# Optimization experiments

Measured on AMD Instinct MI355X. Metric: run time of the kernel, lower is better.

Reference implementation:

```python
import jax, jax.numpy as jnp
import numpy as np

N = 500_000      # number of gaussians
F = 32           # grid feature dim (WavePlaneField.feat_dim)
R = 128          # plane resolution
W = 256          # MLP width
BOUNDS = 1.6     # scene aabb half-extent (args.bounds)


def setup_inputs() -> dict:
    key = jax.random.key(0)
    ks = jax.random.split(key, 16)
    s = lambda d: 1.0 / np.sqrt(d)
    return {
        "rays_pts_emb": jax.random.normal(ks[0], (N, 3), jnp.float32),
        "rotations_emb": jax.random.normal(ks[1], (N, 4), jnp.float32),
        "scale_emb": jax.random.uniform(ks[2], (N, 3), jnp.float32),
        "shs_emb": jax.random.normal(ks[3], (N, 16, 3), jnp.float32),
        "view_dir": jax.random.normal(ks[4], (N, 3), jnp.float32),
        "time_emb": jax.random.uniform(ks[5], (N, 1), jnp.float32),
        "h_emb": jax.random.normal(ks[6], (N, 2), jnp.float32),
        # multiplicative k-planes: init near 1 so products are well-scaled
        "space_planes": 1.0 + 0.1 * jax.random.normal(ks[7], (3, R, R, F), jnp.float32),
        "time_planes": 1.0 + 0.1 * jax.random.normal(ks[8], (3, R, R, F), jnp.float32),
        "w_enc": s(F) * jax.random.normal(ks[9], (F, W), jnp.float32),
        "b_enc": jnp.zeros((W,), jnp.float32),
        "w1": s(W) * jax.random.normal(ks[10], (W, W), jnp.float32),
        "b1": jnp.zeros((W,), jnp.float32),
        "w2": s(W) * jax.random.normal(ks[11], (W, 16 * 3), jnp.float32),
        "b2": jnp.zeros((16 * 3,), jnp.float32),
    }


def _interp2d(plane, u, v):
    """Bilinear sample plane [R,R,F] at normalized coords u,v in [0,1]. -> [N,F]"""
    Rr = plane.shape[0]
    x = jnp.clip(u, 0.0, 1.0) * (Rr - 1)
    y = jnp.clip(v, 0.0, 1.0) * (Rr - 1)
    x0 = jnp.clip(jnp.floor(x), 0, Rr - 2).astype(jnp.int32)
    y0 = jnp.clip(jnp.floor(y), 0, Rr - 2).astype(jnp.int32)
    fx = (x - x0)[:, None]
    fy = (y - y0)[:, None]
    p00 = plane[y0, x0]
    p01 = plane[y0, x0 + 1]
    p10 = plane[y0 + 1, x0]
    p11 = plane[y0 + 1, x0 + 1]
    return (p00 * (1 - fx) + p01 * fx) * (1 - fy) + (p10 * (1 - fx) + p11 * fx) * fy


def _covariance(scale, rotation):
    """3DGS: L = R(q) @ diag(s); cov = L L^T; return 6 unique entries [N,6]."""
    q = rotation / jnp.linalg.norm(rotation, axis=-1, keepdims=True)
    r, x, y, z = q[:, 0], q[:, 1], q[:, 2], q[:, 3]
    Rm = jnp.stack([
        jnp.stack([1 - 2 * (y * y + z * z), 2 * (x * y - r * z), 2 * (x * z + r * y)], -1),
        jnp.stack([2 * (x * y + r * z), 1 - 2 * (x * x + z * z), 2 * (y * z - r * x)], -1),
        jnp.stack([2 * (x * z - r * y), 2 * (y * z + r * x), 1 - 2 * (x * x + y * y)], -1),
    ], axis=1)  # [N,3,3]
    L = Rm * scale[:, None, :]                      # R @ diag(s)
    cov = jnp.einsum('nij,nkj->nik', L, L)          # L @ L^T
    return jnp.stack([cov[:, 0, 0], cov[:, 0, 1], cov[:, 0, 2],
                      cov[:, 1, 1], cov[:, 1, 2], cov[:, 2, 2]], axis=-1)


def reference(rays_pts_emb, rotations_emb, scale_emb, shs_emb, view_dir, time_emb,
              h_emb, space_planes, time_planes, w_enc, b_enc, w1, b1, w2, b2):
    # quaternion -> covariance (passed into grid in original; grid lookup itself
    # only needs positions/time, so symm is computed but unused downstream)
    symm = _covariance(scale_emb, rotations_emb)

    pts = rays_pts_emb[:, :3]
    pn = jnp.clip(pts / BOUNDS, -1.0, 1.0) * 0.5 + 0.5  # aabb-normalize to [0,1]
    xn, yn, zn = pn[:, 0], pn[:, 1], pn[:, 2]
    t = jnp.clip(time_emb[:, 0], 0.0, 1.0)

    space = (_interp2d(space_planes[0], xn, yn)
             * _interp2d(space_planes[1], xn, zn)
             * _interp2d(space_planes[2], yn, zn))          # [N,F]
    spacetime = (_interp2d(time_planes[0], xn, t)
                 * _interp2d(time_planes[1], yn, t)
                 * _interp2d(time_planes[2], zn, t))        # [N,F]

    feat = (space * spacetime) @ w_enc + b_enc              # spacetime_enc (Linear only)
    h = jax.nn.relu(feat) @ w1 + b1                         # shs_deform MLP
    d = jax.nn.relu(h) @ w2 + b2                            # [N,48]
    shs = shs_emb + d.reshape(-1, 16, 3)

    del symm  # original forward discards covariance after grid query
    return (rays_pts_emb, rotations_emb, h_emb[:, 0:1], shs)
```

## Files before the change

### kernel.cpp

```cpp
#include <hip/hip_runtime.h>
#include <hip/hip_fp16.h>

#define NPTS 500000
#define RPLANE 128
#define FDIM 32
#define PLSZ (RPLANE * RPLANE * FDIM)

typedef __bf16 bfx8 __attribute__((ext_vector_type(8)));
typedef float f32x4 __attribute__((ext_vector_type(4)));

__device__ __forceinline__ unsigned short f2bf(float f) {
    unsigned int u = __builtin_bit_cast(unsigned int, f);
    unsigned int r = (u + 0x7FFFu + ((u >> 16) & 1u)) >> 16;
    return (unsigned short)r;
}

__device__ __forceinline__ unsigned pk2(float a, float b) {
    return (unsigned)f2bf(a) | ((unsigned)f2bf(b) << 16);
}

__device__ __forceinline__ __half2 u2h(unsigned u) {
    return __builtin_bit_cast(__half2, u);
}

__device__ __forceinline__ bfx8 asfrag(uint4 v) {
    return __builtin_bit_cast(bfx8, v);
}

__device__ __forceinline__ uint4 convD(unsigned e0, unsigned e1, unsigned o0,
                                       unsigned o1, int a0, int a1, bool sel) {
    uint4 W;
    int x, y;
    x = __builtin_amdgcn_ds_bpermute(a0, (int)e0);
    y = __builtin_amdgcn_ds_bpermute(a0, (int)o0);
    W.x = (unsigned)(sel ? y : x);
    x = __builtin_amdgcn_ds_bpermute(a0, (int)e1);
    y = __builtin_amdgcn_ds_bpermute(a0, (int)o1);
    W.y = (unsigned)(sel ? y : x);
    x = __builtin_amdgcn_ds_bpermute(a1, (int)e0);
    y = __builtin_amdgcn_ds_bpermute(a1, (int)o0);
    W.z = (unsigned)(sel ? y : x);
    x = __builtin_amdgcn_ds_bpermute(a1, (int)e1);
    y = __builtin_amdgcn_ds_bpermute(a1, (int)o1);
    W.w = (unsigned)(sel ? y : x);
    return W;
}

__global__ void prep_all(const float* __restrict__ wenc, const float* __restrict__ w1,
                         const float* __restrict__ w2, const float* __restrict__ spf,
                         const float* __restrict__ tpf,
                         unsigned short* __restrict__ wf, __half* __restrict__ ph) {
    const int WTOT = 86016;
    const int PTOT = 6 * PLSZ;
    const int total = WTOT + PTOT;
    for (int i = blockIdx.x * blockDim.x + threadIdx.x; i < total;
         i += gridDim.x * blockDim.x) {
        if (i < WTOT) {
            const float* W;
            unsigned short* dst;
            int K, Ncols, idx;
            if (i < 8192)       { W = wenc; K = 32;  Ncols = 256; idx = i;         dst = wf; }
            else if (i < 73728) { W = w1;   K = 256; Ncols = 256; idx = i - 8192;  dst = wf + 8192; }
            else                { W = w2;   K = 256; Ncols = 48;  idx = i - 73728; dst = wf + 73728; }
            int j = idx & 7;
            int l = (idx >> 3) & 63;
            int b = idx >> 9;
            int KS = K >> 5;
            int ct = b / KS;
            int ks = b - ct * KS;
            int k = ks * 32 + ((l >> 4) << 3) + j;
            int col = ct * 16 + (l & 15);
            dst[idx] = f2bf(W[(size_t)k * Ncols + col]);
        } else {
            int j = i - WTOT;
            float v = (j < 3 * PLSZ) ? spf[j] : tpf[j - 3 * PLSZ];
            ph[j] = __float2half(v);
        }
    }
}

__global__ void pass_copy(const float* __restrict__ rays, const float* __restrict__ rot,
                          const float* __restrict__ h, float* __restrict__ out) {
    const int total = NPTS * 8;
    for (int i = blockIdx.x * blockDim.x + threadIdx.x; i < total; i += gridDim.x * blockDim.x) {
        float v;
        if (i < NPTS * 3) v = rays[i];
        else if (i < NPTS * 7) v = rot[i - NPTS * 3];
        else v = h[(i - NPTS * 7) * 2];
        out[i] = v;
    }
}

__global__ __launch_bounds__(256, 2) void fused4(
    const float* __restrict__ rays, const float* __restrict__ tme,
    const float* __restrict__ shs, const __half* __restrict__ ph,
    const unsigned short* __restrict__ wf,
    const float* __restrict__ benc, const float* __restrict__ b1v,
    const float* __restrict__ b2v, float* __restrict__ out) {
    const int tid = threadIdx.x;
    const int wid = tid >> 6;
    const int lane = tid & 63;
    const int p0 = blockIdx.x * 128 + wid * 32;
    if (p0 >= NPTS) return;
    const int g = lane >> 4;
    const int c = lane & 15;
    const int f0 = g << 3;
    const int a0 = 4 * (32 * (g & 1) + c);
    const int a1 = a0 + 64;
    const bool sel = (g >> 1) != 0;

    bfx8 act1[2];
#pragma unroll
    for (int pt = 0; pt < 2; ++pt) {
        int p = p0 + pt * 16 + c;
        float px = rays[p * 3 + 0], py = rays[p * 3 + 1], pz = rays[p * 3 + 2];
        const float inv = 0.625f;
        float xn = fminf(fmaxf(px * inv, -1.f), 1.f) * 0.5f + 0.5f;
        float yn = fminf(fmaxf(py * inv, -1.f), 1.f) * 0.5f + 0.5f;
        float zn = fminf(fmaxf(pz * inv, -1.f), 1.f) * 0.5f + 0.5f;
        float tt = fminf(fmaxf(tme[p], 0.f), 1.f);
        float c4[4] = {xn, yn, zn, tt};
        int i0[4];
        float fr[4];
#pragma unroll
        for (int cc = 0; cc < 4; ++cc) {
            float x = c4[cc] * 127.0f;
            float xf = fminf(floorf(x), 126.0f);
            i0[cc] = (int)xf;
            fr[cc] = x - xf;
        }
        const int uc[6] = {0, 0, 1, 0, 1, 2};
        const int vc[6] = {1, 2, 2, 3, 3, 3};
        __half2 g2[4];
#pragma unroll
        for (int pl = 0; pl < 6; ++pl) {
            int x0 = i0[uc[pl]], y0 = i0[vc[pl]];
            float fx = fr[uc[pl]], fy = fr[vc[pl]];
            const __half* base = ph + (size_t)pl * PLSZ + ((y0 * RPLANE + x0) << 5) + f0;
            uint4 q00 = *(const uint4*)base;
            uint4 q01 = *(const uint4*)(base + FDIM);
            uint4 q10 = *(const uint4*)(base + RPLANE * FDIM);
            uint4 q11 = *(const uint4*)(base + RPLANE * FDIM + FDIM);
            __half2 wa = __float2half2_rn((1.f - fx) * (1.f - fy));
            __half2 wb = __float2half2_rn(fx * (1.f - fy));
            __half2 wc = __float2half2_rn((1.f - fx) * fy);
            __half2 wd = __float2half2_rn(fx * fy);
            unsigned qa[4] = {q00.x, q00.y, q00.z, q00.w};
            unsigned qb[4] = {q01.x, q01.y, q01.z, q01.w};
            unsigned qc[4] = {q10.x, q10.y, q10.z, q10.w};
            unsigned qd[4] = {q11.x, q11.y, q11.z, q11.w};
#pragma unroll
            for (int i = 0; i < 4; ++i) {
                __half2 r = __hmul2(u2h(qa[i]), wa);
                r = __hfma2(u2h(qb[i]), wb, r);
                r = __hfma2(u2h(qc[i]), wc, r);
                r = __hfma2(u2h(qd[i]), wd, r);
                g2[i] = (pl == 0) ? r : __hmul2(g2[i], r);
            }
        }
        uint4 av;
        {
            float2 v0 = __half22float2(g2[0]);
            float2 v1 = __half22float2(g2[1]);
            float2 v2 = __half22float2(g2[2]);
            float2 v3 = __half22float2(g2[3]);
            av.x = pk2(v0.x, v0.y);
            av.y = pk2(v1.x, v1.y);
            av.z = pk2(v2.x, v2.y);
            av.w = pk2(v3.x, v3.y);
        }
        act1[pt] = asfrag(av);
    }

    uint4 act2[2][8];
    {
        uint4 wA = *(const uint4*)(wf + 0 * 512 + lane * 8);
        uint4 wB;
        unsigned stE[2][2];
#pragma unroll
        for (int ct = 0; ct < 16; ++ct) {
            uint4 cur = (ct & 1) ? wB : wA;
            if (ct < 15) {
                uint4 nx = *(const uint4*)(wf + (size_t)(ct + 1) * 512 + lane * 8);
                if (ct & 1) wA = nx; else wB = nx;
            }
            float4 b4 = *(const float4*)(benc + 16 * ct + 4 * g);
            float bb[4] = {b4.x, b4.y, b4.z, b4.w};
#pragma unroll
            for (int pt = 0; pt < 2; ++pt) {
                f32x4 z = {0.f, 0.f, 0.f, 0.f};
                f32x4 d = __builtin_amdgcn_mfma_f32_16x16x32_bf16(asfrag(cur), act1[pt], z, 0, 0, 0);
                float v0 = fmaxf(d[0] + bb[0], 0.f);
                float v1 = fmaxf(d[1] + bb[1], 0.f);
                float v2 = fmaxf(d[2] + bb[2], 0.f);
                float v3 = fmaxf(d[3] + bb[3], 0.f);
                unsigned Q0 = pk2(v0, v1), Q1 = pk2(v2, v3);
                if ((ct & 1) == 0) {
                    stE[pt][0] = Q0; stE[pt][1] = Q1;
                } else {
                    act2[pt][ct >> 1] = convD(stE[pt][0], stE[pt][1], Q0, Q1, a0, a1, sel);
                }
            }
        }
    }

    uint4 act3[2][8];
    {
        const unsigned short* w1f = wf + 8192;
        uint4 bufA[8], bufB[8];
#pragma unroll
        for (int ks = 0; ks < 8; ++ks)
            bufA[ks] = *(const uint4*)(w1f + (size_t)ks * 512 + lane * 8);
        unsigned stE[2][2];
#pragma unroll
        for (int ct = 0; ct < 16; ++ct) {
            if (ct < 15) {
#pragma unroll
                for (int ks = 0; ks < 8; ++ks) {
                    uint4 nx = *(const uint4*)(w1f + (size_t)((ct + 1) * 8 + ks) * 512 + lane * 8);
                    if (ct & 1) bufA[ks] = nx; else bufB[ks] = nx;
                }
            }
            float4 b4 = *(const float4*)(b1v + 16 * ct + 4 * g);
            float bb[4] = {b4.x, b4.y, b4.z, b4.w};
#pragma unroll
            for (int pt = 0; pt < 2; ++pt) {
                f32x4 acc = {0.f, 0.f, 0.f, 0.f};
#pragma unroll
                for (int ks = 0; ks < 8; ++ks) {
                    uint4 w = (ct & 1) ? bufB[ks] : bufA[ks];
                    acc = __builtin_amdgcn_mfma_f32_16x16x32_bf16(asfrag(w), asfrag(act2[pt][ks]), acc, 0, 0, 0);
                }
                float v0 = fmaxf(acc[0] + bb[0], 0.f);
                float v1 = fmaxf(acc[1] + bb[1], 0.f);
                float v2 = fmaxf(acc[2] + bb[2], 0.f);
                float v3 = fmaxf(acc[3] + bb[3], 0.f);
                unsigned Q0 = pk2(v0, v1), Q1 = pk2(v2, v3);
                if ((ct & 1) == 0) {
                    stE[pt][0] = Q0; stE[pt][1] = Q1;
                } else {
                    act3[pt][ct >> 1] = convD(stE[pt][0], stE[pt][1], Q0, Q1, a0, a1, sel);
                }
            }
        }
    }

    {
        const unsigned short* w2f = wf + 73728;
#pragma unroll
        for (int ct = 0; ct < 3; ++ct) {
            uint4 wl[8];
#pragma unroll
            for (int ks = 0; ks < 8; ++ks)
                wl[ks] = *(const uint4*)(w2f + (size_t)(ct * 8 + ks) * 512 + lane * 8);
            float bias = b2v[16 * ct + c];
#pragma unroll
            for (int pt = 0; pt < 2; ++pt) {
                f32x4 acc = {0.f, 0.f, 0.f, 0.f};
#pragma unroll
                for (int ks = 0; ks < 8; ++ks)
                    acc = __builtin_amdgcn_mfma_f32_16x16x32_bf16(asfrag(act3[pt][ks]), asfrag(wl[ks]), acc, 0, 0, 0);
#pragma unroll
                for (int r = 0; r < 4; ++r) {
                    int p = p0 + pt * 16 + 4 * g + r;
                    size_t idx = (size_t)p * 48 + 16 * ct + c;
                    out[(size_t)NPTS * 8 + idx] = shs[idx] + acc[r] + bias;
                }
            }
        }
    }
}

extern "C" void kernel_launch(void* const* d_in, const int* in_sizes, int n_in,
                              void* d_out, int out_size, void* d_ws, size_t ws_size,
                              hipStream_t stream) {
    const float* rays = (const float*)d_in[0];
    const float* rot  = (const float*)d_in[1];
    const float* shs  = (const float*)d_in[3];
    const float* tme  = (const float*)d_in[5];
    const float* h_e  = (const float*)d_in[6];
    const float* spf  = (const float*)d_in[7];
    const float* tpf  = (const float*)d_in[8];
    const float* wenc = (const float*)d_in[9];
    const float* benc = (const float*)d_in[10];
    const float* w1   = (const float*)d_in[11];
    const float* b1v  = (const float*)d_in[12];
    const float* w2   = (const float*)d_in[13];
    const float* b2v  = (const float*)d_in[14];
    float* out = (float*)d_out;
    unsigned short* wf = (unsigned short*)d_ws;
    __half* ph = (__half*)(wf + 86016);

    prep_all<<<3408, 256, 0, stream>>>(wenc, w1, w2, spf, tpf, wf, ph);
    pass_copy<<<2048, 256, 0, stream>>>(rays, rot, h_e, out);
    fused4<<<(NPTS + 127) / 128, 256, 0, stream>>>(
        rays, tme, shs, ph, wf, benc, b1v, b2v, out);
}
```

Measured before the change: 236.4 us.

## Stage MLP weights in LDS and run a persistent grid over point tiles

Each block now cooperatively loads W1 and W2 (about 152 KB of bf16) into shared memory once. It then launches a fixed grid of 977 blocks with 512 threads, where each wave handles up to two 32-point tiles. The goal is to stop every wave from re-streaming the weights through global memory and L2. The cost is a large LDS footprint that limits blocks per CU, plus a per-block staging prologue and barrier. Only 977 blocks with two tiles each may also leave parallelism thin for hiding the latency of the plane gathers.

```diff
diff --git a/kernel.cpp b/kernel.cpp
--- a/kernel.cpp
+++ b/kernel.cpp
@@ -5,6 +5,9 @@
 #define RPLANE 128
 #define FDIM 32
 #define PLSZ (RPLANE * RPLANE * FDIM)
+#define NTILES 15625
+#define NBLK 977
+#define TSTRIDE (NBLK * 8)
 
 typedef __bf16 bfx8 __attribute__((ext_vector_type(8)));
 typedef float f32x4 __attribute__((ext_vector_type(4)));
@@ -91,17 +94,22 @@
     }
 }
 
-__global__ __launch_bounds__(256, 2) void fused4(
+__global__ __launch_bounds__(512, 2) void fused5(
     const float* __restrict__ rays, const float* __restrict__ tme,
     const float* __restrict__ shs, const __half* __restrict__ ph,
     const unsigned short* __restrict__ wf,
     const float* __restrict__ benc, const float* __restrict__ b1v,
     const float* __restrict__ b2v, float* __restrict__ out) {
+    __shared__ unsigned short wlds[77824];
     const int tid = threadIdx.x;
     const int wid = tid >> 6;
     const int lane = tid & 63;
-    const int p0 = blockIdx.x * 128 + wid * 32;
-    if (p0 >= NPTS) return;
+
+#pragma unroll
+    for (int i = tid * 8; i < 77824; i += 512 * 8)
+        *(uint4*)&wlds[i] = *(const uint4*)(wf + 8192 + i);
+    __syncthreads();
+
     const int g = lane >> 4;
     const int c = lane & 15;
     const int f0 = g << 3;
@@ -109,162 +117,151 @@
     const int a1 = a0 + 64;
     const bool sel = (g >> 1) != 0;
 
-    bfx8 act1[2];
-#pragma unroll
-    for (int pt = 0; pt < 2; ++pt) {
-        int p = p0 + pt * 16 + c;
-        float px = rays[p * 3 + 0], py = rays[p * 3 + 1], pz = rays[p * 3 + 2];
-        const float inv = 0.625f;
-        float xn = fminf(fmaxf(px * inv, -1.f), 1.f) * 0.5f + 0.5f;
-        float yn = fminf(fmaxf(py * inv, -1.f), 1.f) * 0.5f + 0.5f;
-        float zn = fminf(fmaxf(pz * inv, -1.f), 1.f) * 0.5f + 0.5f;
-        float tt = fminf(fmaxf(tme[p], 0.f), 1.f);
-        float c4[4] = {xn, yn, zn, tt};
-        int i0[4];
-        float fr[4];
-#pragma unroll
-        for (int cc = 0; cc < 4; ++cc) {
-            float x = c4[cc] * 127.0f;
-            float xf = fminf(floorf(x), 126.0f);
-            i0[cc] = (int)xf;
-            fr[cc] = x - xf;
-        }
-        const int uc[6] = {0, 0, 1, 0, 1, 2};
-        const int vc[6] = {1, 2, 2, 3, 3, 3};
-        __half2 g2[4];
-#pragma unroll
-        for (int pl = 0; pl < 6; ++pl) {
-            int x0 = i0[uc[pl]], y0 = i0[vc[pl]];
-            float fx = fr[uc[pl]], fy = fr[vc[pl]];
-            const __half* base = ph + (size_t)pl * PLSZ + ((y0 * RPLANE + x0) << 5) + f0;
-            uint4 q00 = *(const uint4*)base;
-            uint4 q01 = *(const uint4*)(base + FDIM);
-            uint4 q10 = *(const uint4*)(base + RPLANE * FDIM);
-            uint4 q11 = *(const uint4*)(base + RPLANE * FDIM + FDIM);
-            __half2 wa = __float2half2_rn((1.f - fx) * (1.f - fy));
-            __half2 wb = __float2half2_rn(fx * (1.f - fy));
-            __half2 wc = __float2half2_rn((1.f - fx) * fy);
-            __half2 wd = __float2half2_rn(fx * fy);
-            unsigned qa[4] = {q00.x, q00.y, q00.z, q00.w};
-            unsigned qb[4] = {q01.x, q01.y, q01.z, q01.w};
-            unsigned qc[4] = {q10.x, q10.y, q10.z, q10.w};
-            unsigned qd[4] = {q11.x, q11.y, q11.z, q11.w};
-#pragma unroll
-            for (int i = 0; i < 4; ++i) {
-                __half2 r = __hmul2(u2h(qa[i]), wa);
-                r = __hfma2(u2h(qb[i]), wb, r);
-                r = __hfma2(u2h(qc[i]), wc, r);
-                r = __hfma2(u2h(qd[i]), wd, r);
-                g2[i] = (pl == 0) ? r : __hmul2(g2[i], r);
-            }
-        }
-        uint4 av;
+    for (int k = 0; k < 2; ++k) {
+        int tile = blockIdx.x * 8 + wid + k * TSTRIDE;
+        if (tile >= NTILES) continue;
+        const int p0 = tile * 32;
+
+        bfx8 act1[2];
+#pragma unroll
+        for (int pt = 0; pt < 2; ++pt) {
+            int p = p0 + pt * 16 + c;
+            float px = rays[p * 3 + 0], py = rays[p * 3 + 1], pz = rays[p * 3 + 2];
+            const float inv = 0.625f;
+            float xn = fminf(fmaxf(px * inv, -1.f), 1.f) * 0.5f + 0.5f;
+            float yn = fminf(fmaxf(py * inv, -1.f), 1.f) * 0.5f + 0.5f;
+            float zn = fminf(fmaxf(pz * inv, -1.f), 1.f) * 0.5f + 0.5f;
+            float tt = fminf(fmaxf(tme[p], 0.f), 1.f);
+            float c4[4] = {xn, yn, zn, tt};
+            int i0[4];
+            float fr[4];
+#pragma unroll
+            for (int cc = 0; cc < 4; ++cc) {
+                float x = c4[cc] * 127.0f;
+                float xf = fminf(floorf(x), 126.0f);
+                i0[cc] = (int)xf;
+                fr[cc] = x - xf;
+            }
+            const int uc[6] = {0, 0, 1, 0, 1, 2};
+            const int vc[6] = {1, 2, 2, 3, 3, 3};
+            __half2 g2[4];
+#pragma unroll
+            for (int pl = 0; pl < 6; ++pl) {
+                int x0 = i0[uc[pl]], y0 = i0[vc[pl]];
+                float fx = fr[uc[pl]], fy = fr[vc[pl]];
+                const __half* base = ph + (size_t)pl * PLSZ + ((y0 * RPLANE + x0) << 5) + f0;
+                uint4 q00 = *(const uint4*)base;
+                uint4 q01 = *(const uint4*)(base + FDIM);
+                uint4 q10 = *(const uint4*)(base + RPLANE * FDIM);
+                uint4 q11 = *(const uint4*)(base + RPLANE * FDIM + FDIM);
+                __half2 wa = __float2half2_rn((1.f - fx) * (1.f - fy));
+                __half2 wb = __float2half2_rn(fx * (1.f - fy));
+                __half2 wc = __float2half2_rn((1.f - fx) * fy);
+                __half2 wd = __float2half2_rn(fx * fy);
+                unsigned qa[4] = {q00.x, q00.y, q00.z, q00.w};
+                unsigned qb[4] = {q01.x, q01.y, q01.z, q01.w};
+                unsigned qc[4] = {q10.x, q10.y, q10.z, q10.w};
+                unsigned qd[4] = {q11.x, q11.y, q11.z, q11.w};
+#pragma unroll
+                for (int i = 0; i < 4; ++i) {
+                    __half2 r = __hmul2(u2h(qa[i]), wa);
+                    r = __hfma2(u2h(qb[i]), wb, r);
+                    r = __hfma2(u2h(qc[i]), wc, r);
+                    r = __hfma2(u2h(qd[i]), wd, r);
+                    g2[i] = (pl == 0) ? r : __hmul2(g2[i], r);
+                }
+            }
+            uint4 av;
+            {
+                float2 v0 = __half22float2(g2[0]);
+                float2 v1 = __half22float2(g2[1]);
+                float2 v2 = __half22float2(g2[2]);
+                float2 v3 = __half22float2(g2[3]);
+                av.x = pk2(v0.x, v0.y);
+                av.y = pk2(v1.x, v1.y);
+                av.z = pk2(v2.x, v2.y);
+                av.w = pk2(v3.x, v3.y);
+            }
+            act1[pt] = asfrag(av);
+        }
+
+        uint4 act2[2][8];
         {
-            float2 v0 = __half22float2(g2[0]);
-            float2 v1 = __half22float2(g2[1]);
-            float2 v2 = __half22float2(g2[2]);
-            float2 v3 = __half22float2(g2[3]);
-            av.x = pk2(v0.x, v0.y);
-            av.y = pk2(v1.x, v1.y);
-            av.z = pk2(v2.x, v2.y);
-            av.w = pk2(v3.x, v3.y);
-        }
-        act1[pt] = asfrag(av);
-    }
-
-    uint4 act2[2][8];
-    {
-        uint4 wA = *(const uint4*)(wf + 0 * 512 + lane * 8);
-        uint4 wB;
-        unsigned stE[2][2];
-#pragma unroll
-        for (int ct = 0; ct < 16; ++ct) {
-            uint4 cur = (ct & 1) ? wB : wA;
-            if (ct < 15) {
-                uint4 nx = *(const uint4*)(wf + (size_t)(ct + 1) * 512 + lane * 8);
-                if (ct & 1) wA = nx; else wB = nx;
-            }
-            float4 b4 = *(const float4*)(benc + 16 * ct + 4 * g);
-            float bb[4] = {b4.x, b4.y, b4.z, b4.w};
-#pragma unroll
-            for (int pt = 0; pt < 2; ++pt) {
-                f32x4 z = {0.f, 0.f, 0.f, 0.f};
-                f32x4 d = __builtin_amdgcn_mfma_f32_16x16x32_bf16(asfrag(cur), act1[pt], z, 0, 0, 0);
-                float v0 = fmaxf(d[0] + bb[0], 0.f);
-                float v1 = fmaxf(d[1] + bb[1], 0.f);
-                float v2 = fmaxf(d[2] + bb[2], 0.f);
-                float v3 = fmaxf(d[3] + bb[3], 0.f);
-                unsigned Q0 = pk2(v0, v1), Q1 = pk2(v2, v3);
-                if ((ct & 1) == 0) {
-                    stE[pt][0] = Q0; stE[pt][1] = Q1;
-                } else {
-                    act2[pt][ct >> 1] = convD(stE[pt][0], stE[pt][1], Q0, Q1, a0, a1, sel);
-                }
-            }
-        }
-    }
-
-    uint4 act3[2][8];
-    {
-        const unsigned short* w1f = wf + 8192;
-        uint4 bufA[8], bufB[8];
-#pragma unroll
-        for (int ks = 0; ks < 8; ++ks)
-            bufA[ks] = *(const uint4*)(w1f + (size_t)ks * 512 + lane * 8);
-        unsigned stE[2][2];
-#pragma unroll
-        for (int ct = 0; ct < 16; ++ct) {
-            if (ct < 15) {
-#pragma unroll
-                for (int ks = 0; ks < 8; ++ks) {
-                    uint4 nx = *(const uint4*)(w1f + (size_t)((ct + 1) * 8 + ks) * 512 + lane * 8);
-                    if (ct & 1) bufA[ks] = nx; else bufB[ks] = nx;
-                }
-            }
-            float4 b4 = *(const float4*)(b1v + 16 * ct + 4 * g);
-            float bb[4] = {b4.x, b4.y, b4.z, b4.w};
-#pragma unroll
-            for (int pt = 0; pt < 2; ++pt) {
-                f32x4 acc = {0.f, 0.f, 0.f, 0.f};
-#pragma unroll
-                for (int ks = 0; ks < 8; ++ks) {
-                    uint4 w = (ct & 1) ? bufB[ks] : bufA[ks];
-                    acc = __builtin_amdgcn_mfma_f32_16x16x32_bf16(asfrag(w), asfrag(act2[pt][ks]), acc, 0, 0, 0);
-                }
-                float v0 = fmaxf(acc[0] + bb[0], 0.f);
-                float v1 = fmaxf(acc[1] + bb[1], 0.f);
-                float v2 = fmaxf(acc[2] + bb[2], 0.f);
-                float v3 = fmaxf(acc[3] + bb[3], 0.f);
-                unsigned Q0 = pk2(v0, v1), Q1 = pk2(v2, v3);
-                if ((ct & 1) == 0) {
-                    stE[pt][0] = Q0; stE[pt][1] = Q1;
-                } else {
-                    act3[pt][ct >> 1] = convD(stE[pt][0], stE[pt][1], Q0, Q1, a0, a1, sel);
-                }
-            }
-        }
-    }
-
-    {
-        const unsigned short* w2f = wf + 73728;
-#pragma unroll
-        for (int ct = 0; ct < 3; ++ct) {
-            uint4 wl[8];
-#pragma unroll
-            for (int ks = 0; ks < 8; ++ks)
-                wl[ks] = *(const uint4*)(w2f + (size_t)(ct * 8 + ks) * 512 + lane * 8);
-            float bias = b2v[16 * ct + c];
-#pragma unroll
-            for (int pt = 0; pt < 2; ++pt) {
-                f32x4 acc = {0.f, 0.f, 0.f, 0.f};
+            unsigned stE[2][2];
+#pragma unroll
+            for (int ct = 0; ct < 16; ++ct) {
+                uint4 cur = *(const uint4*)(wf + (size_t)ct * 512 + lane * 8);
+                float4 b4 = *(const float4*)(benc + 16 * ct + 4 * g);
+                float bb[4] = {b4.x, b4.y, b4.z, b4.w};
+#pragma unroll
+                for (int pt = 0; pt < 2; ++pt) {
+                    f32x4 z = {0.f, 0.f, 0.f, 0.f};
+                    f32x4 d = __builtin_amdgcn_mfma_f32_16x16x32_bf16(asfrag(cur), act1[pt], z, 0, 0, 0);
+                    float v0 = fmaxf(d[0] + bb[0], 0.f);
+                    float v1 = fmaxf(d[1] + bb[1], 0.f);
+                    float v2 = fmaxf(d[2] + bb[2], 0.f);
+                    float v3 = fmaxf(d[3] + bb[3], 0.f);
+                    unsigned Q0 = pk2(v0, v1), Q1 = pk2(v2, v3);
+                    if ((ct & 1) == 0) {
+                        stE[pt][0] = Q0; stE[pt][1] = Q1;
+                    } else {
+                        act2[pt][ct >> 1] = convD(stE[pt][0], stE[pt][1], Q0, Q1, a0, a1, sel);
+                    }
+                }
+            }
+        }
+
+        uint4 act3[2][8];
+        {
+            unsigned stE[2][2];
+#pragma unroll
+            for (int ct = 0; ct < 16; ++ct) {
+                uint4 w[8];
 #pragma unroll
                 for (int ks = 0; ks < 8; ++ks)
-                    acc = __builtin_amdgcn_mfma_f32_16x16x32_bf16(asfrag(act3[pt][ks]), asfrag(wl[ks]), acc, 0, 0, 0);
-#pragma unroll
-                for (int r = 0; r < 4; ++r) {
-                    int p = p0 + pt * 16 + 4 * g + r;
-                    size_t idx = (size_t)p * 48 + 16 * ct + c;
-                    out[(size_t)NPTS * 8 + idx] = shs[idx] + acc[r] + bias;
+                    w[ks] = *(const uint4*)&wlds[(ct * 8 + ks) * 512 + lane * 8];
+                float4 b4 = *(const float4*)(b1v + 16 * ct + 4 * g);
+                float bb[4] = {b4.x, b4.y, b4.z, b4.w};
+#pragma unroll
+                for (int pt = 0; pt < 2; ++pt) {
+                    f32x4 acc = {0.f, 0.f, 0.f, 0.f};
+#pragma unroll
+                    for (int ks = 0; ks < 8; ++ks)
+                        acc = __builtin_amdgcn_mfma_f32_16x16x32_bf16(asfrag(w[ks]), asfrag(act2[pt][ks]), acc, 0, 0, 0);
+                    float v0 = fmaxf(acc[0] + bb[0], 0.f);
+                    float v1 = fmaxf(acc[1] + bb[1], 0.f);
+                    float v2 = fmaxf(acc[2] + bb[2], 0.f);
+                    float v3 = fmaxf(acc[3] + bb[3], 0.f);
+                    unsigned Q0 = pk2(v0, v1), Q1 = pk2(v2, v3);
+                    if ((ct & 1) == 0) {
+                        stE[pt][0] = Q0; stE[pt][1] = Q1;
+                    } else {
+                        act3[pt][ct >> 1] = convD(stE[pt][0], stE[pt][1], Q0, Q1, a0, a1, sel);
+                    }
+                }
+            }
+        }
+
+        {
+#pragma unroll
+            for (int ct = 0; ct < 3; ++ct) {
+                uint4 wl[8];
+#pragma unroll
+                for (int ks = 0; ks < 8; ++ks)
+                    wl[ks] = *(const uint4*)&wlds[65536 + (ct * 8 + ks) * 512 + lane * 8];
+                float bias = b2v[16 * ct + c];
+#pragma unroll
+                for (int pt = 0; pt < 2; ++pt) {
+                    f32x4 acc = {0.f, 0.f, 0.f, 0.f};
+#pragma unroll
+                    for (int ks = 0; ks < 8; ++ks)
+                        acc = __builtin_amdgcn_mfma_f32_16x16x32_bf16(asfrag(act3[pt][ks]), asfrag(wl[ks]), acc, 0, 0, 0);
+#pragma unroll
+                    for (int r = 0; r < 4; ++r) {
+                        int p = p0 + pt * 16 + 4 * g + r;
+                        size_t idx = (size_t)p * 48 + 16 * ct + c;
+                        out[(size_t)NPTS * 8 + idx] = shs[idx] + acc[r] + bias;
+                    }
                 }
             }
         }
@@ -293,6 +290,6 @@
 
     prep_all<<<3408, 256, 0, stream>>>(wenc, w1, w2, spf, tpf, wf, ph);
     pass_copy<<<2048, 256, 0, stream>>>(rays, rot, h_e, out);
-    fused4<<<(NPTS + 127) / 128, 256, 0, stream>>>(
+    fused5<<<NBLK, 512, 0, stream>>>(
         rays, tme, shs, ph, wf, benc, b1v, b2v, out);
 }
```

Result: faster. 207.3 us (-12.3%).
